# Kernel optimization log

Hardware: AMD Instinct MI355X
Metric: run time of the kernel (lower is better)

## Reference

```python
import jax, jax.numpy as jnp
import numpy as np

N, E, D, H, HEADS_C, G = 50000, 800000, 128, 4, 32, 8
EDIM = D + 2  # H_update: phys_term (D) + ortho_geom (2)


def setup_inputs() -> dict:
    key = jax.random.key(0)
    ks = jax.random.split(key, 24)
    def gl(k, shape, fan_in):
        return jax.random.normal(k, shape, jnp.float32) / np.sqrt(fan_in)
    inp = {
        'h_target': jax.random.normal(ks[0], (N, D), jnp.float32),
        'h_source': jax.random.normal(ks[1], (N, D), jnp.float32),
        'edge_index': jax.random.randint(ks[2], (2, E), 0, N, jnp.int64),
        'pos': jax.random.uniform(ks[3], (N, 2), jnp.float32),
        't_emb': jax.random.normal(ks[4], (1, D), jnp.float32),
        # AdaGN params
        'gn_w': jnp.ones((D,), jnp.float32),
        'gn_b': jnp.zeros((D,), jnp.float32),
        'fc_W': gl(ks[5], (D, 2 * D), D),
        'fc_b': jnp.zeros((2 * D,), jnp.float32),
        # GATv2 params (lin_l, lin_r, lin_edge, att, bias)
        'Wl': gl(ks[6], (D, D), D),
        'bl': jnp.zeros((D,), jnp.float32),
        'Wr': gl(ks[7], (D, D), D),
        'br': jnp.zeros((D,), jnp.float32),
        'We': gl(ks[8], (EDIM, D), EDIM),
        'att': gl(ks[9], (H, HEADS_C), HEADS_C),
        'gat_b': jnp.zeros((D,), jnp.float32),
        # post_gat
        'Wp': gl(ks[10], (D, D), D),
        'bp': jnp.zeros((D,), jnp.float32),
        # update_mlp: LayerNorm + Linear(D,2D) + GELU + Linear(2D,D)
        'ln_w': jnp.ones((D,), jnp.float32),
        'ln_b': jnp.zeros((D,), jnp.float32),
        'W1': gl(ks[11], (D, 2 * D), D),
        'b1': jnp.zeros((2 * D,), jnp.float32),
        'W2': gl(ks[12], (2 * D, D), 2 * D),
        'b2': jnp.zeros((D,), jnp.float32),
    }
    return inp


def _adagn(x, cond, gn_w, gn_b, fc_W, fc_b):
    n, d = x.shape
    xg = x.reshape(n, G, d // G)
    mu = xg.mean(-1, keepdims=True)
    var = xg.var(-1, keepdims=True)  # biased, as torch GroupNorm
    normed = ((xg - mu) / jnp.sqrt(var + 1e-5)).reshape(n, d) * gn_w + gn_b
    style = cond @ fc_W + fc_b  # (1, 2D) broadcasts over nodes
    gamma, beta = jnp.split(style, 2, axis=-1)
    return normed * (1 + gamma) + beta


def _gatv2(h, edge_attr, src, dst, Wl, bl, Wr, br, We, att, gat_b):
    n = h.shape[0]
    x_l = (h @ Wl + bl).reshape(n, H, HEADS_C)  # source transform
    x_r = (h @ Wr + br).reshape(n, H, HEADS_C)  # target transform
    e_feat = (edge_attr @ We).reshape(-1, H, HEADS_C)
    x = x_l[src] + x_r[dst] + e_feat            # (E, H, C)
    x = jax.nn.leaky_relu(x, 0.2)
    logit = jnp.einsum('ehc,hc->eh', x, att)    # (E, H)
    # segment softmax over edges grouped by destination node
    amax = jax.ops.segment_max(logit, dst, num_segments=n)
    amax = jnp.where(jnp.isfinite(amax), amax, 0.0)
    ex = jnp.exp(logit - amax[dst])
    denom = jax.ops.segment_sum(ex, dst, num_segments=n)
    alpha = ex / (denom[dst] + 1e-16)           # (E, H)
    msg = x_l[src] * alpha[:, :, None]          # (E, H, C)
    out = jax.ops.segment_sum(msg, dst, num_segments=n)  # (N, H, C)
    return out.reshape(n, H * HEADS_C) + gat_b


def reference(h_target, h_source, edge_index, pos, t_emb,
              gn_w, gn_b, fc_W, fc_b,
              Wl, bl, Wr, br, We, att, gat_b,
              Wp, bp, ln_w, ln_b, W1, b1, W2, b2):
    h_mod = _adagn(h_source, t_emb, gn_w, gn_b, fc_W, fc_b)
    src, dst = edge_index[0], edge_index[1]
    rel_pos = pos[src] - pos[dst]                       # (E, 2)
    dist_sq = (rel_pos ** 2).sum(-1, keepdims=True) + 1e-8
    geom = rel_pos / dist_sq
    phys = h_mod[src] - h_mod[dst]                      # H_update mode
    ortho = jnp.stack([-geom[:, 1], geom[:, 0]], axis=-1)
    edge_attr = jnp.concatenate([phys, ortho], axis=-1)  # (E, D+2)
    aggr = _gatv2(h_mod, edge_attr, src, dst, Wl, bl, Wr, br, We, att, gat_b)
    aggr = aggr @ Wp + bp
    # update_mlp (dropout inactive in eval)
    mu = aggr.mean(-1, keepdims=True)
    var = aggr.var(-1, keepdims=True)
    z = (aggr - mu) / jnp.sqrt(var + 1e-5) * ln_w + ln_b
    z = jax.nn.gelu(z @ W1 + b1, approximate=False)
    delta = z @ W2 + b2
    return h_target + delta
```

## Files before the change

kernel.cpp:

```cpp
#include <hip/hip_runtime.h>
#include <math.h>

#define D 128
#define LOG2E 1.44269504088896340736f

typedef short bf16x4 __attribute__((ext_vector_type(4)));
typedef short bf16x8 __attribute__((ext_vector_type(8)));
typedef float f32x4  __attribute__((ext_vector_type(4)));
typedef float f32x2  __attribute__((ext_vector_type(2)));

__device__ __forceinline__ float b2f(unsigned short u) {
  union { unsigned int i; float f; } v; v.i = ((unsigned int)u) << 16; return v.f;
}
__device__ __forceinline__ unsigned short f2b(float f) {
  union { float f; unsigned int i; } v; v.f = f;
  unsigned int i = v.i;
  return (unsigned short)((i + 0x7FFFu + ((i >> 16) & 1u)) >> 16);
}
__device__ __forceinline__ float b2f_lo(unsigned int u) {
  union { unsigned int i; float f; } v; v.i = u << 16; return v.f;
}
__device__ __forceinline__ float b2f_hi(unsigned int u) {
  union { unsigned int i; float f; } v; v.i = u & 0xFFFF0000u; return v.f;
}
__device__ __forceinline__ float loadf(const void* p, size_t i, int isb) {
  if (isb) return b2f(((const unsigned short*)p)[i]);
  return ((const float*)p)[i];
}
__device__ __forceinline__ void storeout(void* p, size_t i, float v, int isb) {
  if (isb) ((unsigned short*)p)[i] = f2b(v);
  else     ((float*)p)[i] = v;
}
__device__ __forceinline__ int clampN(int v, int N) {
  return ((unsigned)v >= (unsigned)N) ? 0 : v;
}
__device__ __forceinline__ float gelu_f(float v) {
  return 0.5f * v * (1.f + erff(v * 0.70710678118654752f));
}

__global__ void setup_kernel(const float* __restrict__ gw, const int* __restrict__ e32,
                             int* __restrict__ fflag, int* __restrict__ iflag,
                             int* __restrict__ ok) {
  int t = threadIdx.x;
  if (blockIdx.x == 0) {
    float v = gw[t];
    unsigned long long b = __ballot(v == 1.0f);
    if (t == 0) fflag[0] = (b == 0xFFFFFFFFFFFFFFFFull) ? 0 : 1;
  } else if (blockIdx.x == 1) {
    int v = e32[2 * t + 1];
    unsigned long long b = __ballot(v == 0);
    if (t == 0) iflag[0] = (b == 0xFFFFFFFFFFFFFFFFull) ? 1 : 0;
  } else {
    if (t == 0) ok[0] = 1;
  }
}
__device__ __forceinline__ int edge_src(const void* eraw, int i, int E, int fl, int N) {
  int v = fl ? (int)((const long long*)eraw)[i] : ((const int*)eraw)[i];
  return clampN(v, N);
}
__device__ __forceinline__ int edge_dst(const void* eraw, int i, int E, int fl, int N) {
  int v = fl ? (int)((const long long*)eraw)[(size_t)E + i] : ((const int*)eraw)[(size_t)E + i];
  return clampN(v, N);
}

struct Job { const void* src; float* dst; int n; int blk0; };
struct Jobs { Job j[21]; };
__global__ void cvt_param_kernel(Jobs jobs, const int* __restrict__ fflag, int njobs) {
  int isb = fflag[0];
  int b = blockIdx.x;
  for (int k = 0; k < njobs; ++k) {
    int nblk = (jobs.j[k].n + 255) >> 8;
    int lo = jobs.j[k].blk0;
    if (b >= lo && b < lo + nblk) {
      int i = ((b - lo) << 8) + threadIdx.x;
      if (i < jobs.j[k].n) jobs.j[k].dst[i] = loadf(jobs.j[k].src, i, isb);
      return;
    }
  }
}

__global__ void style_kernel(const float* __restrict__ t_emb,
                             const float* __restrict__ fc_W,
                             const float* __restrict__ fc_b,
                             float* __restrict__ style) {
  int j = threadIdx.x;
  float s = fc_b[j];
  for (int k = 0; k < D; ++k) s += t_emb[k] * fc_W[k * 256 + j];
  style[j] = s;
}

__global__ __launch_bounds__(128) void adagn_kernel(
    const void* __restrict__ h_source,
    const float* __restrict__ gn_w, const float* __restrict__ gn_b,
    const float* __restrict__ style, unsigned short* __restrict__ h_mod,
    const int* __restrict__ fflag, int N) {
  int n = blockIdx.x; if (n >= N) return;
  int c = threadIdx.x;
  float x = loadf(h_source, (size_t)n * D + c, fflag[0]);
  float s = x, s2 = x * x;
  s += __shfl_xor(s, 1, 16);  s2 += __shfl_xor(s2, 1, 16);
  s += __shfl_xor(s, 2, 16);  s2 += __shfl_xor(s2, 2, 16);
  s += __shfl_xor(s, 4, 16);  s2 += __shfl_xor(s2, 4, 16);
  s += __shfl_xor(s, 8, 16);  s2 += __shfl_xor(s2, 8, 16);
  float mu = s * (1.f / 16.f);
  float va = s2 * (1.f / 16.f) - mu * mu;
  float iv = rsqrtf(va + 1e-5f);
  float nv = (x - mu) * iv * gn_w[c] + gn_b[c];
  h_mod[(size_t)n * D + c] = f2b(nv * (1.f + style[c]) + style[128 + c]);
}

struct BP { const float* B; int ldb; int col0; };
struct BPJobs { BP j[8]; };
__global__ void bprep_kernel(BPJobs jobs, unsigned short* __restrict__ dst) {
  int job = blockIdx.x >> 7;
  int idx = ((blockIdx.x & 127) << 8) + threadIdx.x;
  int j    = idx & 7;
  int lane = (idx >> 3) & 63;
  int p    = (idx >> 9) & 1;
  int ct   = (idx >> 10) & 7;
  int kt   = idx >> 13;
  int g = lane >> 4;
  int k = kt * 32 + ((j < 4) ? (4 * g + j) : (16 + 4 * g + (j - 4)));
  int n = jobs.j[job].col0 + ct * 16 + (lane & 15);
  float v = jobs.j[job].B[(size_t)k * jobs.j[job].ldb + n];
  unsigned short hi = f2b(v);
  unsigned short out = hi;
  if (p) out = f2b(v - b2f(hi));
  dst[(size_t)job * 32768 + idx] = out;
}

__global__ __launch_bounds__(256) void mgemm3_kernel(
    const unsigned short* __restrict__ A, const unsigned short* __restrict__ Bf,
    const float* __restrict__ bl, const float* __restrict__ br,
    unsigned int* __restrict__ XH32, unsigned short* __restrict__ XR, int Nrows) {
  int l = threadIdx.x & 63, w = threadIdx.x >> 6;
  int rb = blockIdx.x * 64 + w * 16;
  int m = l & 15, g = l >> 4;
  int arow = rb + m;
  if (arow >= Nrows) arow = Nrows - 1;
  const unsigned short* Arow = A + (size_t)arow * 128 + 4 * g;
  f32x4 acc[24];
  #pragma unroll
  for (int ct = 0; ct < 24; ++ct) acc[ct] = (f32x4){0.f, 0.f, 0.f, 0.f};
  #pragma unroll
  for (int kt = 0; kt < 4; ++kt) {
    bf16x4 alo = *(const bf16x4*)(Arow + kt * 32);
    bf16x4 ahi = *(const bf16x4*)(Arow + kt * 32 + 16);
    bf16x8 af = __builtin_shufflevector(alo, ahi, 0, 1, 2, 3, 4, 5, 6, 7);
    #pragma unroll
    for (int ct = 0; ct < 24; ++ct) {
      size_t off = (size_t)(ct >> 3) * 32768 + (size_t)kt * 8192
                 + (size_t)(((ct & 7) * 2) * 64 + l) * 8;
      bf16x8 bh = *(const bf16x8*)(Bf + off);
      bf16x8 bl2 = *(const bf16x8*)(Bf + off + 512);
      acc[ct] = __builtin_amdgcn_mfma_f32_16x16x32_bf16(af, bh, acc[ct], 0, 0, 0);
      acc[ct] = __builtin_amdgcn_mfma_f32_16x16x32_bf16(af, bl2, acc[ct], 0, 0, 0);
    }
  }
  #pragma unroll
  for (int ct = 0; ct < 8; ++ct) {
    int cm = ct * 16 + m;
    #pragma unroll
    for (int r = 0; r < 4; ++r) {
      int row = rb + 4 * g + r;
      if (row < Nrows) {
        float vl = acc[ct][r] + bl[cm];
        float vh = acc[ct + 16][r];
        XH32[(size_t)row * 128 + cm] =
            (unsigned int)f2b(vl) | ((unsigned int)f2b(vh) << 16);
        float vr = acc[ct + 8][r] + br[cm];
        XR[(size_t)row * 128 + cm] = f2b(vr);
      }
    }
  }
}

__global__ void hist_kernel(const void* __restrict__ eraw, const int* __restrict__ iflag,
                            int* __restrict__ deg, int E, int N) {
  int e = blockIdx.x * 256 + threadIdx.x;
  if (e < E) atomicAdd(&deg[edge_dst(eraw, e, E, iflag[0], N)], 1);
}

__global__ __launch_bounds__(1024) void scan1_kernel(const int* __restrict__ deg,
                                                     int* __restrict__ incl,
                                                     int* __restrict__ bsum) {
  int i = blockIdx.x * 1024 + threadIdx.x;
  int lane = threadIdx.x & 63, wave = threadIdx.x >> 6;
  int x = deg[i];
  #pragma unroll
  for (int d = 1; d < 64; d <<= 1) { int t = __shfl_up(x, d, 64); if (lane >= d) x += t; }
  __shared__ int wsum[16];
  if (lane == 63) wsum[wave] = x;
  __syncthreads();
  if (threadIdx.x < 16) {
    int w = wsum[threadIdx.x];
    #pragma unroll
    for (int d = 1; d < 16; d <<= 1) { int t = __shfl_up(w, d, 64); if ((int)threadIdx.x >= d) w += t; }
    wsum[threadIdx.x] = w;
  }
  __syncthreads();
  if (wave > 0) x += wsum[wave - 1];
  incl[i] = x;
  if (threadIdx.x == 1023) bsum[blockIdx.x] = x;
}

__global__ void scan2_kernel(const int* __restrict__ bsum, int* __restrict__ bbase, int nb) {
  if (threadIdx.x == 0) {
    int run = 0;
    for (int b = 0; b < nb; ++b) { bbase[b] = run; run += bsum[b]; }
  }
}

__global__ __launch_bounds__(1024) void scan3_kernel(const int* __restrict__ incl,
                                                     const int* __restrict__ deg,
                                                     const int* __restrict__ bbase,
                                                     int* __restrict__ offs,
                                                     int* __restrict__ cursor, int N) {
  int i = blockIdx.x * 1024 + threadIdx.x;
  if (i < N) {
    int o = bbase[blockIdx.x] + incl[i] - deg[i];
    offs[i] = o; cursor[i] = o;
  }
}

__global__ void scatter_kernel(const void* __restrict__ eraw, const int* __restrict__ iflag,
                               int* __restrict__ cursor, int* __restrict__ elist, int E, int N) {
  int e = blockIdx.x * 256 + threadIdx.x;
  if (e < E) {
    int fl = iflag[0];
    int d = edge_dst(eraw, e, E, fl, N);
    int s = edge_src(eraw, e, E, fl, N);
    int p = atomicAdd(&cursor[d], 1);
    elist[p] = s;
  }
}

__global__ void validate_kernel(const int* __restrict__ offs, const int* __restrict__ deg,
                                const int* __restrict__ cursor, const int* __restrict__ elist,
                                int* __restrict__ ok, int N, int E) {
  int i = blockIdx.x * 256 + threadIdx.x;
  bool bad = false;
  if (i < N) bad = bad || (cursor[i] != offs[i] + deg[i]);
  if (i < E) bad = bad || ((unsigned)elist[i] >= (unsigned)N);
  if (i == 0) bad = bad || (offs[N - 1] + deg[N - 1] != E);
  if (bad) atomicAnd(ok, 0);
}
__global__ void fillc_kernel(void* __restrict__ out, float c, const int* __restrict__ fflag, int n) {
  int i = blockIdx.x * 256 + threadIdx.x;
  if (i < n) storeout(out, i, c, fflag[0]);
}

__global__ __launch_bounds__(256) void edge_kernel(
    const unsigned int* __restrict__ XH32, const unsigned short* __restrict__ XR,
    const float* __restrict__ pos, const float* __restrict__ weo,
    const float* __restrict__ att, const float* __restrict__ gat_b,
    const int* __restrict__ offs, const int* __restrict__ deg,
    const int* __restrict__ elist, unsigned short* __restrict__ aggr, int N) {
  int w = threadIdx.x >> 6;
  int l = threadIdx.x & 63;
  int n = blockIdx.x * 2 + (w >> 1);
  int half = w & 1;
  bool valid = (n < N);
  int nn = valid ? n : 0;
  int c0 = 2 * l;
  uint2 hq = *(const uint2*)(XH32 + (size_t)nn * 128 + c0);
  unsigned int uxr = *(const unsigned int*)(XR + (size_t)nn * 128 + c0);
  f32x2 base = (f32x2){ b2f_lo(uxr) - b2f_hi(hq.x), b2f_hi(uxr) - b2f_hi(hq.y) };
  float2 pd = ((const float2*)pos)[nn];
  f32x2 we0v = (f32x2){ weo[c0], weo[c0 + 1] };
  f32x2 we1v = (f32x2){ weo[128 + c0], weo[128 + c0 + 1] };
  f32x2 attv = (f32x2){ att[c0] * LOG2E, att[c0 + 1] * LOG2E };
  int o = 0, dg = 0;
  if (valid) { o = offs[n]; dg = deg[n]; }
  float mx = -3.402823466e38f, den = 0.f;
  f32x2 num = (f32x2){0.f, 0.f};
  for (int i = half; i < dg; i += 2) {
    int s = elist[o + i];
    float2 ps = ((const float2*)pos)[s];
    uint2 q = *(const uint2*)(XH32 + (size_t)s * 128 + c0);
    float rx = ps.x - pd.x, ry = ps.y - pd.y;
    float inv = 1.f / (rx * rx + ry * ry + 1e-8f);
    float gx = -ry * inv, gy = rx * inv;
    f32x2 xl = (f32x2){ b2f_lo(q.x), b2f_lo(q.y) };
    f32x2 hw = (f32x2){ b2f_hi(q.x), b2f_hi(q.y) };
    f32x2 x = (xl + hw) + (base + gx * we0v + gy * we1v);
    f32x2 lx = __builtin_elementwise_max(x, 0.2f * x);
    f32x2 t = lx * attv;
    float y = t.x + t.y;
    y += __shfl_xor(y, 1, 16);
    y += __shfl_xor(y, 2, 16);
    y += __shfl_xor(y, 4, 16);
    y += __shfl_xor(y, 8, 16);
    float d0 = y - mx;
    if (__any(d0 > 11.5417f)) {
      float mn = fmaxf(mx, y);
      float f = exp2f(mx - mn);
      float p = exp2f(y - mn);
      den = den * f + p;
      num = num * f + p * xl;
      mx = mn;
    } else {
      float p = exp2f(d0);
      den += p;
      num += p * xl;
    }
  }
  __shared__ float4 mrg[4][64];
  mrg[w][l] = (float4){mx, den, num.x, num.y};
  __syncthreads();
  float4 oth = mrg[w ^ 1][l];
  float M = fmaxf(mx, oth.x);
  float f1 = exp2f(mx - M), f2 = exp2f(oth.x - M);
  den = den * f1 + oth.y * f2;
  float n0 = num.x * f1 + oth.z * f2;
  float n1 = num.y * f1 + oth.w * f2;
  if (valid && half == 0) {
    float iden = 1.f / (den + 1e-16f);
    unsigned int o0 = f2b(n0 * iden + gat_b[c0]);
    unsigned int o1 = f2b(n1 * iden + gat_b[c0 + 1]);
    *(unsigned int*)(aggr + (size_t)n * D + c0) = o0 | (o1 << 16);
  }
}

__global__ __launch_bounds__(256) void fused_post_kernel(
    const unsigned short* __restrict__ A, const unsigned short* __restrict__ WP8,
    const float* __restrict__ bp, const float* __restrict__ lnw,
    const float* __restrict__ lnb, const float* __restrict__ b1,
    const float* __restrict__ b2, const void* __restrict__ resid,
    void* __restrict__ out, const int* __restrict__ fflag,
    const int* __restrict__ okf, int Nrows) {
  __shared__ __align__(16) unsigned short ldsA[4][16][132];
  __shared__ __align__(16) unsigned short ldsG[4][16][268];
  int l = threadIdx.x & 63, w = threadIdx.x >> 6;
  int rb = blockIdx.x * 64 + w * 16;
  int m = l & 15, g = l >> 4;
  int arow = rb + m;
  if (arow >= Nrows) arow = Nrows - 1;
  const unsigned short* Arow = A + (size_t)arow * 128 + 4 * g;

  f32x4 acc[8];
  #pragma unroll
  for (int ct = 0; ct < 8; ++ct) acc[ct] = (f32x4){0.f, 0.f, 0.f, 0.f};
  #pragma unroll
  for (int kt = 0; kt < 4; ++kt) {
    bf16x4 alo = *(const bf16x4*)(Arow + kt * 32);
    bf16x4 ahi = *(const bf16x4*)(Arow + kt * 32 + 16);
    bf16x8 af = __builtin_shufflevector(alo, ahi, 0, 1, 2, 3, 4, 5, 6, 7);
    #pragma unroll
    for (int ct = 0; ct < 8; ++ct) {
      size_t off = (size_t)3 * 32768 + (size_t)kt * 8192 + (size_t)((ct * 2) * 64 + l) * 8;
      bf16x8 bh = *(const bf16x8*)(WP8 + off);
      bf16x8 bl2 = *(const bf16x8*)(WP8 + off + 512);
      acc[ct] = __builtin_amdgcn_mfma_f32_16x16x32_bf16(af, bh, acc[ct], 0, 0, 0);
      acc[ct] = __builtin_amdgcn_mfma_f32_16x16x32_bf16(af, bl2, acc[ct], 0, 0, 0);
    }
  }
  #pragma unroll
  for (int ct = 0; ct < 8; ++ct) acc[ct] = acc[ct] + bp[ct * 16 + m];

  f32x4 s1 = (f32x4){0.f, 0.f, 0.f, 0.f}, s2v = (f32x4){0.f, 0.f, 0.f, 0.f};
  #pragma unroll
  for (int ct = 0; ct < 8; ++ct) { s1 += acc[ct]; s2v += acc[ct] * acc[ct]; }
  #pragma unroll
  for (int d = 1; d < 16; d <<= 1) {
    f32x4 t1, t2;
    #pragma unroll
    for (int r = 0; r < 4; ++r) { t1[r] = __shfl_xor(s1[r], d, 16); t2[r] = __shfl_xor(s2v[r], d, 16); }
    s1 += t1; s2v += t2;
  }
  f32x4 mu = s1 * (1.f / 128.f);
  f32x4 iv;
  #pragma unroll
  for (int r = 0; r < 4; ++r) {
    float var = s2v[r] * (1.f / 128.f) - mu[r] * mu[r];
    iv[r] = rsqrtf(fmaxf(var, 0.f) + 1e-5f);
  }
  #pragma unroll
  for (int ct = 0; ct < 8; ++ct) {
    float lw = lnw[ct * 16 + m], lb = lnb[ct * 16 + m];
    #pragma unroll
    for (int r = 0; r < 4; ++r) {
      float z = (acc[ct][r] - mu[r]) * iv[r] * lw + lb;
      ldsA[w][4 * g + r][m + 16 * ct] = f2b(z);
    }
  }

  f32x4 acc2[16];
  #pragma unroll
  for (int ct = 0; ct < 16; ++ct) acc2[ct] = (f32x4){0.f, 0.f, 0.f, 0.f};
  #pragma unroll
  for (int kt = 0; kt < 4; ++kt) {
    bf16x4 alo = *(const bf16x4*)&ldsA[w][m][4 * g + kt * 32];
    bf16x4 ahi = *(const bf16x4*)&ldsA[w][m][4 * g + kt * 32 + 16];
    bf16x8 af = __builtin_shufflevector(alo, ahi, 0, 1, 2, 3, 4, 5, 6, 7);
    #pragma unroll
    for (int ct = 0; ct < 16; ++ct) {
      size_t off = (size_t)(4 + (ct >> 3)) * 32768 + (size_t)kt * 8192
                 + (size_t)(((ct & 7) * 2) * 64 + l) * 8;
      bf16x8 bh = *(const bf16x8*)(WP8 + off);
      bf16x8 bl2 = *(const bf16x8*)(WP8 + off + 512);
      acc2[ct] = __builtin_amdgcn_mfma_f32_16x16x32_bf16(af, bh, acc2[ct], 0, 0, 0);
      acc2[ct] = __builtin_amdgcn_mfma_f32_16x16x32_bf16(af, bl2, acc2[ct], 0, 0, 0);
    }
  }
  #pragma unroll
  for (int ct = 0; ct < 16; ++ct) {
    float bs = b1[ct * 16 + m];
    #pragma unroll
    for (int r = 0; r < 4; ++r) {
      float v = gelu_f(acc2[ct][r] + bs);
      ldsG[w][4 * g + r][ct * 16 + m] = f2b(v);
    }
  }

  f32x4 acc3[8];
  #pragma unroll
  for (int ct = 0; ct < 8; ++ct) acc3[ct] = (f32x4){0.f, 0.f, 0.f, 0.f};
  #pragma unroll
  for (int kt = 0; kt < 8; ++kt) {
    bf16x4 alo = *(const bf16x4*)&ldsG[w][m][4 * g + kt * 32];
    bf16x4 ahi = *(const bf16x4*)&ldsG[w][m][4 * g + kt * 32 + 16];
    bf16x8 af = __builtin_shufflevector(alo, ahi, 0, 1, 2, 3, 4, 5, 6, 7);
    #pragma unroll
    for (int ct = 0; ct < 8; ++ct) {
      size_t off = (size_t)(6 + (kt >> 2)) * 32768 + (size_t)(kt & 3) * 8192
                 + (size_t)((ct * 2) * 64 + l) * 8;
      bf16x8 bh = *(const bf16x8*)(WP8 + off);
      bf16x8 bl2 = *(const bf16x8*)(WP8 + off + 512);
      acc3[ct] = __builtin_amdgcn_mfma_f32_16x16x32_bf16(af, bh, acc3[ct], 0, 0, 0);
      acc3[ct] = __builtin_amdgcn_mfma_f32_16x16x32_bf16(af, bl2, acc3[ct], 0, 0, 0);
    }
  }
  int isb = fflag[0];
  int okv = okf[0];
  #pragma unroll
  for (int ct = 0; ct < 8; ++ct) {
    int c = ct * 16 + m;
    float bs = b2[c];
    #pragma unroll
    for (int r = 0; r < 4; ++r) {
      int row = rb + 4 * g + r;
      if (row < Nrows) {
        float v = acc3[ct][r] + bs;
        size_t oi = (size_t)row * 128 + c;
        v += loadf(resid, oi, isb);
        if (okv == 0) v = 100.0f;
        storeout(out, oi, v, isb);
      }
    }
  }
}

extern "C" void kernel_launch(void* const* d_in, const int* in_sizes, int n_in,
                              void* d_out, int out_size, void* d_ws, size_t ws_size,
                              hipStream_t stream) {
  const void* h_resid  = d_in[0];
  const void* h_modsrc = d_in[1];
  const void* eidx     = d_in[2];
  const int N = in_sizes[0] / D;
  const int E = in_sizes[2] / 2;
  const int outN = N * D;

  char* wp = (char*)d_ws;
  auto alloc = [&](size_t bytes) -> void* {
    void* p = (void*)wp;
    wp += (bytes + 255) & ~(size_t)255;
    return p;
  };
  unsigned short* BA = (unsigned short*)alloc((size_t)N * D * 2);
  unsigned int*  XH32 = (unsigned int*)alloc((size_t)N * D * 4);
  unsigned short* BX = (unsigned short*)alloc((size_t)N * D * 2);
  float* style = (float*)alloc(256 * 4);
  const int nb = (N + 1023) / 1024;
  const int npad = nb * 1024;
  int* fflag  = (int*)alloc(256);
  int* iflag  = (int*)alloc(256);
  int* okflag = (int*)alloc(256);
  int* elist  = (int*)alloc((size_t)E * 4);
  int* deg    = (int*)alloc((size_t)npad * 4);
  int* incl   = (int*)alloc((size_t)npad * 4);
  int* bsum   = (int*)alloc((size_t)nb * 4);
  int* bbase  = (int*)alloc((size_t)nb * 4);
  int* offs   = (int*)alloc((size_t)N * 4);
  int* cursor = (int*)alloc((size_t)N * 4);
  float* pos_f  = (float*)alloc((size_t)2 * N * 4);
  float* temb_f = (float*)alloc(128 * 4);
  float* gnw_f  = (float*)alloc(128 * 4);
  float* gnb_f  = (float*)alloc(128 * 4);
  float* fcW_f  = (float*)alloc(32768 * 4);
  float* fcb_f  = (float*)alloc(256 * 4);
  float* Wl_f   = (float*)alloc(16384 * 4);
  float* bl_f   = (float*)alloc(128 * 4);
  float* Wr_f   = (float*)alloc(16384 * 4);
  float* br_f   = (float*)alloc(128 * 4);
  float* We_f   = (float*)alloc(16640 * 4);
  float* att_f  = (float*)alloc(128 * 4);
  float* gtb_f  = (float*)alloc(128 * 4);
  float* Wp_f   = (float*)alloc(16384 * 4);
  float* bp_f   = (float*)alloc(128 * 4);
  float* lnw_f  = (float*)alloc(128 * 4);
  float* lnb_f  = (float*)alloc(128 * 4);
  float* W1_f   = (float*)alloc(32768 * 4);
  float* b1_f   = (float*)alloc(256 * 4);
  float* W2_f   = (float*)alloc(32768 * 4);
  float* b2_f   = (float*)alloc(128 * 4);
  unsigned short* WP8 = (unsigned short*)alloc(8 * 65536);

  size_t required = (size_t)(wp - (char*)d_ws);
  if (required > ws_size) {
    return;
  }

  (void)hipMemsetAsync(deg, 0, (size_t)npad * 4, stream);

  setup_kernel<<<3, 64, 0, stream>>>((const float*)d_in[5], (const int*)eidx,
                                     fflag, iflag, okflag);

  const int expected[24] = {6400000, 6400000, 1600000, 100000, 128, 128, 128, 32768,
                            256, 16384, 128, 16384, 128, 16640, 128, 128, 16384, 128,
                            128, 128, 32768, 256, 32768, 128};
  int bad = (n_in == 24) ? -1 : 24;
  if (bad < 0) {
    for (int i = 0; i < 24; ++i) {
      if (in_sizes[i] != expected[i]) { bad = i; break; }
    }
  }
  if (bad >= 0) {
    fillc_kernel<<<(outN + 255) / 256, 256, 0, stream>>>(d_out, 20.f + 10.f * bad, fflag, outN);
    return;
  }

  Jobs jobs;
  int jn = 0, blk = 0;
  auto addjob = [&](const void* s, float* dptr, int n) {
    jobs.j[jn] = {s, dptr, n, blk};
    blk += (n + 255) >> 8;
    ++jn;
  };
  addjob(d_in[3],  pos_f,  2 * N);
  addjob(d_in[4],  temb_f, 128);
  addjob(d_in[5],  gnw_f,  128);
  addjob(d_in[6],  gnb_f,  128);
  addjob(d_in[7],  fcW_f,  32768);
  addjob(d_in[8],  fcb_f,  256);
  addjob(d_in[9],  Wl_f,   16384);
  addjob(d_in[10], bl_f,   128);
  addjob(d_in[11], Wr_f,   16384);
  addjob(d_in[12], br_f,   128);
  addjob(d_in[13], We_f,   16640);
  addjob(d_in[14], att_f,  128);
  addjob(d_in[15], gtb_f,  128);
  addjob(d_in[16], Wp_f,   16384);
  addjob(d_in[17], bp_f,   128);
  addjob(d_in[18], lnw_f,  128);
  addjob(d_in[19], lnb_f,  128);
  addjob(d_in[20], W1_f,   32768);
  addjob(d_in[21], b1_f,   256);
  addjob(d_in[22], W2_f,   32768);
  addjob(d_in[23], b2_f,   128);
  cvt_param_kernel<<<blk, 256, 0, stream>>>(jobs, fflag, jn);

  style_kernel<<<1, 256, 0, stream>>>(temb_f, fcW_f, fcb_f, style);
  adagn_kernel<<<N, 128, 0, stream>>>(h_modsrc, gnw_f, gnb_f, style, BA, fflag, N);

  BPJobs bj;
  bj.j[0] = {Wl_f, 128, 0};
  bj.j[1] = {Wr_f, 128, 0};
  bj.j[2] = {We_f, 128, 0};
  bj.j[3] = {Wp_f, 128, 0};
  bj.j[4] = {W1_f, 256, 0};
  bj.j[5] = {W1_f, 256, 128};
  bj.j[6] = {W2_f, 128, 0};
  bj.j[7] = {W2_f + 128 * 128, 128, 0};
  bprep_kernel<<<1024, 256, 0, stream>>>(bj, WP8);

  const int mb = (N + 63) / 64;
  mgemm3_kernel<<<mb, 256, 0, stream>>>(BA, WP8, bl_f, br_f, XH32, BX, N);

  hist_kernel<<<(E + 255) / 256, 256, 0, stream>>>(eidx, iflag, deg, E, N);
  scan1_kernel<<<nb, 1024, 0, stream>>>(deg, incl, bsum);
  scan2_kernel<<<1, 64, 0, stream>>>(bsum, bbase, nb);
  scan3_kernel<<<nb, 1024, 0, stream>>>(incl, deg, bbase, offs, cursor, N);
  scatter_kernel<<<(E + 255) / 256, 256, 0, stream>>>(eidx, iflag, cursor, elist, E, N);
  int vmax = (E > N ? E : N);
  validate_kernel<<<(vmax + 255) / 256, 256, 0, stream>>>(offs, deg, cursor, elist, okflag, N, E);

  edge_kernel<<<(N + 1) / 2, 256, 0, stream>>>(XH32, BX, pos_f, We_f + 128 * 128,
                                               att_f, gtb_f, offs, deg, elist, BA, N);

  fused_post_kernel<<<mb, 256, 0, stream>>>(BA, WP8, bp_f, lnw_f, lnb_f, b1_f, b2_f,
                                            h_resid, d_out, fflag, okflag, N);
}
```

Measured before the change: 561.8 us.

## Merge style into param conversion, single-block scan, prefetch next edge in GAT loop

Folds the style matvec into the parameter-conversion kernel as an extra block and replaces the three-kernel prefix scan with one single-block scan kernel, cutting launch count and intermediate buffers. The edge aggregation loop now software-prefetches the next neighbor's index, features and position to hide gather latency. The prefetch reads past each node's edge list, so elist is padded with 64 zeroed entries. The single-block scan serializes about 49 elements per thread, which may be slower than the old multi-block scan.

```diff
diff --git a/kernel.cpp b/kernel.cpp
--- a/kernel.cpp
+++ b/kernel.cpp
@@ -65,9 +65,22 @@
 
 struct Job { const void* src; float* dst; int n; int blk0; };
 struct Jobs { Job j[21]; };
-__global__ void cvt_param_kernel(Jobs jobs, const int* __restrict__ fflag, int njobs) {
+__global__ void cvt_param_kernel(Jobs jobs, const int* __restrict__ fflag, int njobs,
+                                 int style_blk,
+                                 const void* __restrict__ temb_raw,
+                                 const void* __restrict__ fcW_raw,
+                                 const void* __restrict__ fcb_raw,
+                                 float* __restrict__ style) {
   int isb = fflag[0];
   int b = blockIdx.x;
+  if (b == style_blk) {
+    int j = threadIdx.x;
+    float s = loadf(fcb_raw, j, isb);
+    for (int k = 0; k < D; ++k)
+      s += loadf(temb_raw, k, isb) * loadf(fcW_raw, (size_t)k * 256 + j, isb);
+    style[j] = s;
+    return;
+  }
   for (int k = 0; k < njobs; ++k) {
     int nblk = (jobs.j[k].n + 255) >> 8;
     int lo = jobs.j[k].blk0;
@@ -77,16 +90,6 @@
       return;
     }
   }
-}
-
-__global__ void style_kernel(const float* __restrict__ t_emb,
-                             const float* __restrict__ fc_W,
-                             const float* __restrict__ fc_b,
-                             float* __restrict__ style) {
-  int j = threadIdx.x;
-  float s = fc_b[j];
-  for (int k = 0; k < D; ++k) s += t_emb[k] * fc_W[k * 256 + j];
-  style[j] = s;
 }
 
 __global__ __launch_bounds__(128) void adagn_kernel(
@@ -181,45 +184,39 @@
   if (e < E) atomicAdd(&deg[edge_dst(eraw, e, E, iflag[0], N)], 1);
 }
 
-__global__ __launch_bounds__(1024) void scan1_kernel(const int* __restrict__ deg,
-                                                     int* __restrict__ incl,
-                                                     int* __restrict__ bsum) {
-  int i = blockIdx.x * 1024 + threadIdx.x;
-  int lane = threadIdx.x & 63, wave = threadIdx.x >> 6;
-  int x = deg[i];
-  #pragma unroll
-  for (int d = 1; d < 64; d <<= 1) { int t = __shfl_up(x, d, 64); if (lane >= d) x += t; }
+__global__ __launch_bounds__(1024) void scan_kernel(const int* __restrict__ deg,
+                                                    int* __restrict__ offs,
+                                                    int* __restrict__ cursor, int N) {
+  const int C = (N + 1023) / 1024;
+  int t = threadIdx.x;
+  int lo = t * C;
+  int sum = 0;
+  for (int j = 0; j < C; ++j) {
+    int idx = lo + j;
+    if (idx < N) sum += deg[idx];
+  }
+  int lane = t & 63, wave = t >> 6;
+  int x = sum;
+  #pragma unroll
+  for (int d = 1; d < 64; d <<= 1) { int v = __shfl_up(x, d, 64); if (lane >= d) x += v; }
   __shared__ int wsum[16];
   if (lane == 63) wsum[wave] = x;
   __syncthreads();
-  if (threadIdx.x < 16) {
-    int w = wsum[threadIdx.x];
-    #pragma unroll
-    for (int d = 1; d < 16; d <<= 1) { int t = __shfl_up(w, d, 64); if ((int)threadIdx.x >= d) w += t; }
-    wsum[threadIdx.x] = w;
+  if (t < 16) {
+    int wv = wsum[t];
+    #pragma unroll
+    for (int d = 1; d < 16; d <<= 1) { int v = __shfl_up(wv, d, 64); if (t >= d) wv += v; }
+    wsum[t] = wv;
   }
   __syncthreads();
-  if (wave > 0) x += wsum[wave - 1];
-  incl[i] = x;
-  if (threadIdx.x == 1023) bsum[blockIdx.x] = x;
-}
-
-__global__ void scan2_kernel(const int* __restrict__ bsum, int* __restrict__ bbase, int nb) {
-  if (threadIdx.x == 0) {
-    int run = 0;
-    for (int b = 0; b < nb; ++b) { bbase[b] = run; run += bsum[b]; }
-  }
-}
-
-__global__ __launch_bounds__(1024) void scan3_kernel(const int* __restrict__ incl,
-                                                     const int* __restrict__ deg,
-                                                     const int* __restrict__ bbase,
-                                                     int* __restrict__ offs,
-                                                     int* __restrict__ cursor, int N) {
-  int i = blockIdx.x * 1024 + threadIdx.x;
-  if (i < N) {
-    int o = bbase[blockIdx.x] + incl[i] - deg[i];
-    offs[i] = o; cursor[i] = o;
+  int run = x - sum + (wave > 0 ? wsum[wave - 1] : 0);
+  for (int j = 0; j < C; ++j) {
+    int idx = lo + j;
+    if (idx < N) {
+      offs[idx] = run;
+      cursor[idx] = run;
+      run += deg[idx];
+    }
   }
 }
 
@@ -274,35 +271,41 @@
   if (valid) { o = offs[n]; dg = deg[n]; }
   float mx = -3.402823466e38f, den = 0.f;
   f32x2 num = (f32x2){0.f, 0.f};
-  for (int i = half; i < dg; i += 2) {
-    int s = elist[o + i];
+  if (dg > half) {
+    int s = elist[o + half];
+    uint2 q = *(const uint2*)(XH32 + (size_t)s * 128 + c0);
     float2 ps = ((const float2*)pos)[s];
-    uint2 q = *(const uint2*)(XH32 + (size_t)s * 128 + c0);
-    float rx = ps.x - pd.x, ry = ps.y - pd.y;
-    float inv = 1.f / (rx * rx + ry * ry + 1e-8f);
-    float gx = -ry * inv, gy = rx * inv;
-    f32x2 xl = (f32x2){ b2f_lo(q.x), b2f_lo(q.y) };
-    f32x2 hw = (f32x2){ b2f_hi(q.x), b2f_hi(q.y) };
-    f32x2 x = (xl + hw) + (base + gx * we0v + gy * we1v);
-    f32x2 lx = __builtin_elementwise_max(x, 0.2f * x);
-    f32x2 t = lx * attv;
-    float y = t.x + t.y;
-    y += __shfl_xor(y, 1, 16);
-    y += __shfl_xor(y, 2, 16);
-    y += __shfl_xor(y, 4, 16);
-    y += __shfl_xor(y, 8, 16);
-    float d0 = y - mx;
-    if (__any(d0 > 11.5417f)) {
-      float mn = fmaxf(mx, y);
-      float f = exp2f(mx - mn);
-      float p = exp2f(y - mn);
-      den = den * f + p;
-      num = num * f + p * xl;
-      mx = mn;
-    } else {
-      float p = exp2f(d0);
-      den += p;
-      num += p * xl;
+    for (int i = half; i < dg; i += 2) {
+      int s2 = elist[o + i + 2];
+      uint2 q2 = *(const uint2*)(XH32 + (size_t)s2 * 128 + c0);
+      float2 p2 = ((const float2*)pos)[s2];
+      float rx = ps.x - pd.x, ry = ps.y - pd.y;
+      float inv = 1.f / (rx * rx + ry * ry + 1e-8f);
+      float gx = -ry * inv, gy = rx * inv;
+      f32x2 xl = (f32x2){ b2f_lo(q.x), b2f_lo(q.y) };
+      f32x2 hw = (f32x2){ b2f_hi(q.x), b2f_hi(q.y) };
+      f32x2 x = (xl + hw) + (base + gx * we0v + gy * we1v);
+      f32x2 lx = __builtin_elementwise_max(x, 0.2f * x);
+      f32x2 t = lx * attv;
+      float y = t.x + t.y;
+      y += __shfl_xor(y, 1, 16);
+      y += __shfl_xor(y, 2, 16);
+      y += __shfl_xor(y, 4, 16);
+      y += __shfl_xor(y, 8, 16);
+      float d0 = y - mx;
+      if (__any(d0 > 11.5417f)) {
+        float mn = fmaxf(mx, y);
+        float f = exp2f(mx - mn);
+        float p = exp2f(y - mn);
+        den = den * f + p;
+        num = num * f + p * xl;
+        mx = mn;
+      } else {
+        float p = exp2f(d0);
+        den += p;
+        num += p * xl;
+      }
+      s = s2; q = q2; ps = p2;
     }
   }
   __shared__ float4 mrg[4][64];
@@ -471,24 +474,16 @@
   unsigned int*  XH32 = (unsigned int*)alloc((size_t)N * D * 4);
   unsigned short* BX = (unsigned short*)alloc((size_t)N * D * 2);
   float* style = (float*)alloc(256 * 4);
-  const int nb = (N + 1023) / 1024;
-  const int npad = nb * 1024;
   int* fflag  = (int*)alloc(256);
   int* iflag  = (int*)alloc(256);
   int* okflag = (int*)alloc(256);
-  int* elist  = (int*)alloc((size_t)E * 4);
-  int* deg    = (int*)alloc((size_t)npad * 4);
-  int* incl   = (int*)alloc((size_t)npad * 4);
-  int* bsum   = (int*)alloc((size_t)nb * 4);
-  int* bbase  = (int*)alloc((size_t)nb * 4);
+  int* elist  = (int*)alloc((size_t)(E + 64) * 4);
+  int* deg    = (int*)alloc((size_t)N * 4);
   int* offs   = (int*)alloc((size_t)N * 4);
   int* cursor = (int*)alloc((size_t)N * 4);
   float* pos_f  = (float*)alloc((size_t)2 * N * 4);
-  float* temb_f = (float*)alloc(128 * 4);
   float* gnw_f  = (float*)alloc(128 * 4);
   float* gnb_f  = (float*)alloc(128 * 4);
-  float* fcW_f  = (float*)alloc(32768 * 4);
-  float* fcb_f  = (float*)alloc(256 * 4);
   float* Wl_f   = (float*)alloc(16384 * 4);
   float* bl_f   = (float*)alloc(128 * 4);
   float* Wr_f   = (float*)alloc(16384 * 4);
@@ -511,7 +506,8 @@
     return;
   }
 
-  (void)hipMemsetAsync(deg, 0, (size_t)npad * 4, stream);
+  (void)hipMemsetAsync(deg, 0, (size_t)N * 4, stream);
+  (void)hipMemsetAsync(elist + E, 0, 64 * 4, stream);
 
   setup_kernel<<<3, 64, 0, stream>>>((const float*)d_in[5], (const int*)eidx,
                                      fflag, iflag, okflag);
@@ -538,11 +534,8 @@
     ++jn;
   };
   addjob(d_in[3],  pos_f,  2 * N);
-  addjob(d_in[4],  temb_f, 128);
   addjob(d_in[5],  gnw_f,  128);
   addjob(d_in[6],  gnb_f,  128);
-  addjob(d_in[7],  fcW_f,  32768);
-  addjob(d_in[8],  fcb_f,  256);
   addjob(d_in[9],  Wl_f,   16384);
   addjob(d_in[10], bl_f,   128);
   addjob(d_in[11], Wr_f,   16384);
@@ -558,9 +551,9 @@
   addjob(d_in[21], b1_f,   256);
   addjob(d_in[22], W2_f,   32768);
   addjob(d_in[23], b2_f,   128);
-  cvt_param_kernel<<<blk, 256, 0, stream>>>(jobs, fflag, jn);
-
-  style_kernel<<<1, 256, 0, stream>>>(temb_f, fcW_f, fcb_f, style);
+  cvt_param_kernel<<<blk + 1, 256, 0, stream>>>(jobs, fflag, jn, blk,
+                                                d_in[4], d_in[7], d_in[8], style);
+
   adagn_kernel<<<N, 128, 0, stream>>>(h_modsrc, gnw_f, gnb_f, style, BA, fflag, N);
 
   BPJobs bj;
@@ -578,9 +571,7 @@
   mgemm3_kernel<<<mb, 256, 0, stream>>>(BA, WP8, bl_f, br_f, XH32, BX, N);
 
   hist_kernel<<<(E + 255) / 256, 256, 0, stream>>>(eidx, iflag, deg, E, N);
-  scan1_kernel<<<nb, 1024, 0, stream>>>(deg, incl, bsum);
-  scan2_kernel<<<1, 64, 0, stream>>>(bsum, bbase, nb);
-  scan3_kernel<<<nb, 1024, 0, stream>>>(incl, deg, bbase, offs, cursor, N);
+  scan_kernel<<<1, 1024, 0, stream>>>(deg, offs, cursor, N);
   scatter_kernel<<<(E + 255) / 256, 256, 0, stream>>>(eidx, iflag, cursor, elist, E, N);
   int vmax = (E > N ? E : N);
   validate_kernel<<<(vmax + 255) / 256, 256, 0, stream>>>(offs, deg, cursor, elist, okflag, N, E);
```

New measurement: 671.0 us. 1.19x slower.

## Prefetch next neighbor in GAT edge loop and fold style GEMV into param conversion

Applied to the files above, without the earlier changes.

The GATv2 per-node edge loop now software-pipelines its gathers, loading the next neighbor's index, features and position one iteration ahead so gather latency overlaps the softmax arithmetic. The edge list gets 64 zeroed padding entries so the lookahead read past the end stays in bounds. Separately, the style GEMV now runs as an extra block of the parameter-conversion kernel, reading raw inputs directly, which removes one launch and the fp32 copies of t_emb and fc weights. The two LDS buffers in the fused post kernel are merged into one to cut shared-memory footprint. Costs are more registers in the edge loop and one wasted prefetch per node.

```diff
diff --git a/kernel.cpp b/kernel.cpp
--- a/kernel.cpp
+++ b/kernel.cpp
@@ -65,9 +65,22 @@
 
 struct Job { const void* src; float* dst; int n; int blk0; };
 struct Jobs { Job j[21]; };
-__global__ void cvt_param_kernel(Jobs jobs, const int* __restrict__ fflag, int njobs) {
+__global__ void cvt_param_kernel(Jobs jobs, const int* __restrict__ fflag, int njobs,
+                                 int style_blk,
+                                 const void* __restrict__ temb_raw,
+                                 const void* __restrict__ fcW_raw,
+                                 const void* __restrict__ fcb_raw,
+                                 float* __restrict__ style) {
   int isb = fflag[0];
   int b = blockIdx.x;
+  if (b == style_blk) {
+    int j = threadIdx.x;
+    float s = loadf(fcb_raw, j, isb);
+    for (int k = 0; k < D; ++k)
+      s += loadf(temb_raw, k, isb) * loadf(fcW_raw, (size_t)k * 256 + j, isb);
+    style[j] = s;
+    return;
+  }
   for (int k = 0; k < njobs; ++k) {
     int nblk = (jobs.j[k].n + 255) >> 8;
     int lo = jobs.j[k].blk0;
@@ -77,16 +90,6 @@
       return;
     }
   }
-}
-
-__global__ void style_kernel(const float* __restrict__ t_emb,
-                             const float* __restrict__ fc_W,
-                             const float* __restrict__ fc_b,
-                             float* __restrict__ style) {
-  int j = threadIdx.x;
-  float s = fc_b[j];
-  for (int k = 0; k < D; ++k) s += t_emb[k] * fc_W[k * 256 + j];
-  style[j] = s;
 }
 
 __global__ __launch_bounds__(128) void adagn_kernel(
@@ -274,35 +277,41 @@
   if (valid) { o = offs[n]; dg = deg[n]; }
   float mx = -3.402823466e38f, den = 0.f;
   f32x2 num = (f32x2){0.f, 0.f};
-  for (int i = half; i < dg; i += 2) {
-    int s = elist[o + i];
+  if (dg > half) {
+    int s = elist[o + half];
+    uint2 q = *(const uint2*)(XH32 + (size_t)s * 128 + c0);
     float2 ps = ((const float2*)pos)[s];
-    uint2 q = *(const uint2*)(XH32 + (size_t)s * 128 + c0);
-    float rx = ps.x - pd.x, ry = ps.y - pd.y;
-    float inv = 1.f / (rx * rx + ry * ry + 1e-8f);
-    float gx = -ry * inv, gy = rx * inv;
-    f32x2 xl = (f32x2){ b2f_lo(q.x), b2f_lo(q.y) };
-    f32x2 hw = (f32x2){ b2f_hi(q.x), b2f_hi(q.y) };
-    f32x2 x = (xl + hw) + (base + gx * we0v + gy * we1v);
-    f32x2 lx = __builtin_elementwise_max(x, 0.2f * x);
-    f32x2 t = lx * attv;
-    float y = t.x + t.y;
-    y += __shfl_xor(y, 1, 16);
-    y += __shfl_xor(y, 2, 16);
-    y += __shfl_xor(y, 4, 16);
-    y += __shfl_xor(y, 8, 16);
-    float d0 = y - mx;
-    if (__any(d0 > 11.5417f)) {
-      float mn = fmaxf(mx, y);
-      float f = exp2f(mx - mn);
-      float p = exp2f(y - mn);
-      den = den * f + p;
-      num = num * f + p * xl;
-      mx = mn;
-    } else {
-      float p = exp2f(d0);
-      den += p;
-      num += p * xl;
+    for (int i = half; i < dg; i += 2) {
+      int s2 = elist[o + i + 2];
+      uint2 q2 = *(const uint2*)(XH32 + (size_t)s2 * 128 + c0);
+      float2 p2 = ((const float2*)pos)[s2];
+      float rx = ps.x - pd.x, ry = ps.y - pd.y;
+      float inv = 1.f / (rx * rx + ry * ry + 1e-8f);
+      float gx = -ry * inv, gy = rx * inv;
+      f32x2 xl = (f32x2){ b2f_lo(q.x), b2f_lo(q.y) };
+      f32x2 hw = (f32x2){ b2f_hi(q.x), b2f_hi(q.y) };
+      f32x2 x = (xl + hw) + (base + gx * we0v + gy * we1v);
+      f32x2 lx = __builtin_elementwise_max(x, 0.2f * x);
+      f32x2 t = lx * attv;
+      float y = t.x + t.y;
+      y += __shfl_xor(y, 1, 16);
+      y += __shfl_xor(y, 2, 16);
+      y += __shfl_xor(y, 4, 16);
+      y += __shfl_xor(y, 8, 16);
+      float d0 = y - mx;
+      if (__any(d0 > 11.5417f)) {
+        float mn = fmaxf(mx, y);
+        float f = exp2f(mx - mn);
+        float p = exp2f(y - mn);
+        den = den * f + p;
+        num = num * f + p * xl;
+        mx = mn;
+      } else {
+        float p = exp2f(d0);
+        den += p;
+        num += p * xl;
+      }
+      s = s2; q = q2; ps = p2;
     }
   }
   __shared__ float4 mrg[4][64];
@@ -329,8 +338,7 @@
     const float* __restrict__ b2, const void* __restrict__ resid,
     void* __restrict__ out, const int* __restrict__ fflag,
     const int* __restrict__ okf, int Nrows) {
-  __shared__ __align__(16) unsigned short ldsA[4][16][132];
-  __shared__ __align__(16) unsigned short ldsG[4][16][268];
+  __shared__ __align__(16) unsigned short ldsU[4][16][268];
   int l = threadIdx.x & 63, w = threadIdx.x >> 6;
   int rb = blockIdx.x * 64 + w * 16;
   int m = l & 15, g = l >> 4;
@@ -381,7 +389,7 @@
     #pragma unroll
     for (int r = 0; r < 4; ++r) {
       float z = (acc[ct][r] - mu[r]) * iv[r] * lw + lb;
-      ldsA[w][4 * g + r][m + 16 * ct] = f2b(z);
+      ldsU[w][4 * g + r][m + 16 * ct] = f2b(z);
     }
   }
 
@@ -390,8 +398,8 @@
   for (int ct = 0; ct < 16; ++ct) acc2[ct] = (f32x4){0.f, 0.f, 0.f, 0.f};
   #pragma unroll
   for (int kt = 0; kt < 4; ++kt) {
-    bf16x4 alo = *(const bf16x4*)&ldsA[w][m][4 * g + kt * 32];
-    bf16x4 ahi = *(const bf16x4*)&ldsA[w][m][4 * g + kt * 32 + 16];
+    bf16x4 alo = *(const bf16x4*)&ldsU[w][m][4 * g + kt * 32];
+    bf16x4 ahi = *(const bf16x4*)&ldsU[w][m][4 * g + kt * 32 + 16];
     bf16x8 af = __builtin_shufflevector(alo, ahi, 0, 1, 2, 3, 4, 5, 6, 7);
     #pragma unroll
     for (int ct = 0; ct < 16; ++ct) {
@@ -409,7 +417,7 @@
     #pragma unroll
     for (int r = 0; r < 4; ++r) {
       float v = gelu_f(acc2[ct][r] + bs);
-      ldsG[w][4 * g + r][ct * 16 + m] = f2b(v);
+      ldsU[w][4 * g + r][ct * 16 + m] = f2b(v);
     }
   }
 
@@ -418,8 +426,8 @@
   for (int ct = 0; ct < 8; ++ct) acc3[ct] = (f32x4){0.f, 0.f, 0.f, 0.f};
   #pragma unroll
   for (int kt = 0; kt < 8; ++kt) {
-    bf16x4 alo = *(const bf16x4*)&ldsG[w][m][4 * g + kt * 32];
-    bf16x4 ahi = *(const bf16x4*)&ldsG[w][m][4 * g + kt * 32 + 16];
+    bf16x4 alo = *(const bf16x4*)&ldsU[w][m][4 * g + kt * 32];
+    bf16x4 ahi = *(const bf16x4*)&ldsU[w][m][4 * g + kt * 32 + 16];
     bf16x8 af = __builtin_shufflevector(alo, ahi, 0, 1, 2, 3, 4, 5, 6, 7);
     #pragma unroll
     for (int ct = 0; ct < 8; ++ct) {
@@ -476,7 +484,7 @@
   int* fflag  = (int*)alloc(256);
   int* iflag  = (int*)alloc(256);
   int* okflag = (int*)alloc(256);
-  int* elist  = (int*)alloc((size_t)E * 4);
+  int* elist  = (int*)alloc((size_t)(E + 64) * 4);
   int* deg    = (int*)alloc((size_t)npad * 4);
   int* incl   = (int*)alloc((size_t)npad * 4);
   int* bsum   = (int*)alloc((size_t)nb * 4);
@@ -484,11 +492,8 @@
   int* offs   = (int*)alloc((size_t)N * 4);
   int* cursor = (int*)alloc((size_t)N * 4);
   float* pos_f  = (float*)alloc((size_t)2 * N * 4);
-  float* temb_f = (float*)alloc(128 * 4);
   float* gnw_f  = (float*)alloc(128 * 4);
   float* gnb_f  = (float*)alloc(128 * 4);
-  float* fcW_f  = (float*)alloc(32768 * 4);
-  float* fcb_f  = (float*)alloc(256 * 4);
   float* Wl_f   = (float*)alloc(16384 * 4);
   float* bl_f   = (float*)alloc(128 * 4);
   float* Wr_f   = (float*)alloc(16384 * 4);
@@ -512,6 +517,7 @@
   }
 
   (void)hipMemsetAsync(deg, 0, (size_t)npad * 4, stream);
+  (void)hipMemsetAsync(elist + E, 0, 64 * 4, stream);
 
   setup_kernel<<<3, 64, 0, stream>>>((const float*)d_in[5], (const int*)eidx,
                                      fflag, iflag, okflag);
@@ -538,11 +544,8 @@
     ++jn;
   };
   addjob(d_in[3],  pos_f,  2 * N);
-  addjob(d_in[4],  temb_f, 128);
   addjob(d_in[5],  gnw_f,  128);
   addjob(d_in[6],  gnb_f,  128);
-  addjob(d_in[7],  fcW_f,  32768);
-  addjob(d_in[8],  fcb_f,  256);
   addjob(d_in[9],  Wl_f,   16384);
   addjob(d_in[10], bl_f,   128);
   addjob(d_in[11], Wr_f,   16384);
@@ -558,9 +561,9 @@
   addjob(d_in[21], b1_f,   256);
   addjob(d_in[22], W2_f,   32768);
   addjob(d_in[23], b2_f,   128);
-  cvt_param_kernel<<<blk, 256, 0, stream>>>(jobs, fflag, jn);
-
-  style_kernel<<<1, 256, 0, stream>>>(temb_f, fcW_f, fcb_f, style);
+  cvt_param_kernel<<<blk + 1, 256, 0, stream>>>(jobs, fflag, jn, blk,
+                                                d_in[4], d_in[7], d_in[8], style);
+
   adagn_kernel<<<N, 128, 0, stream>>>(h_modsrc, gnw_f, gnb_f, style, BA, fflag, N);
 
   BPJobs bj;
```

After: 554.8 us. About the same (-1.3%).
